# Performance work log

Hardware: AMD Instinct MI355X
Metric: run time of the kernel (lower is better)

Reference implementation:

```python
import jax, jax.numpy as jnp
import numpy as np

N_OBJ, N_REL = 2048, 32768
OBJ_DIM, POOL, H, E, C = 4096, 2048, 512, 200, 151
GEO = 128
IMG_W, IMG_H = 1024.0, 768.0
NUM_ITER = 3


def _lin(x, W, b):
    return x @ W.T + b


def _gru(x, h, Wih, Whh, bih, bhh):
    # torch.nn.GRUCell math; gates stacked (r, z, n)
    gi = x @ Wih.T + bih
    gh = h @ Whh.T + bhh
    i_r, i_z, i_n = jnp.split(gi, 3, axis=-1)
    h_r, h_z, h_n = jnp.split(gh, 3, axis=-1)
    r = jax.nn.sigmoid(i_r + h_r)
    z = jax.nn.sigmoid(i_z + h_z)
    n = jnp.tanh(i_n + r * h_n)
    return (1.0 - z) * n + z * h


def _box_info(boxes, norm=None):
    # [x1,y1,x2,y2,cx,cy,w,h]
    wh = boxes[:, 2:4] - boxes[:, 0:2] + 1.0
    ctr = boxes[:, 0:2] + 0.5 * wh
    info = jnp.concatenate([boxes, ctr, wh], axis=1)
    return info / norm if norm is not None else info


def _box_pair_info(b1, b2):
    # b1,b2: [R,8] normalized box infos -> [R,32]
    ub = jnp.stack([jnp.minimum(b1[:, 0], b2[:, 0]), jnp.minimum(b1[:, 1], b2[:, 1]),
                    jnp.maximum(b1[:, 2], b2[:, 2]), jnp.maximum(b1[:, 3], b2[:, 3])], axis=1)
    ib = jnp.stack([jnp.maximum(b1[:, 0], b2[:, 0]), jnp.maximum(b1[:, 1], b2[:, 1]),
                    jnp.minimum(b1[:, 2], b2[:, 2]), jnp.minimum(b1[:, 3], b2[:, 3])], axis=1)
    inter = _box_info(ib)
    bad = (ib[:, 2] < ib[:, 0]) | (ib[:, 3] < ib[:, 1])
    inter = jnp.where(bad[:, None], 0.0, inter)
    return jnp.concatenate([b1, b2, _box_info(ub), inter], axis=1)


def _encode_box_info(boxes):
    # motifs 9-d geometry encoding
    wh = boxes[:, 2:4] - boxes[:, 0:2] + 1.0
    xy = boxes[:, 0:2] + 0.5 * wh
    w, h = wh[:, 0:1], wh[:, 1:2]
    x, y = xy[:, 0:1], xy[:, 1:2]
    x1, y1, x2, y2 = boxes[:, 0:1], boxes[:, 1:2], boxes[:, 2:3], boxes[:, 3:4]
    return jnp.concatenate([w / IMG_W, h / IMG_H, x / IMG_W, y / IMG_H, x1 / IMG_W,
                            y1 / IMG_H, x2 / IMG_W, y2 / IMG_H, w * h / (IMG_W * IMG_H)], axis=1)


def _forward(inst_roi_feats, union_features, boxes, emb_dist_W, emb_label_W, up_W, up_b,
             pairup_W, pairup_b, pos1_W, pos1_b, bn_g, bn_b, bn_m, bn_v, pos2_W, pos2_b,
             spt1_W, spt1_b, spt2_W, spt2_b, pairfin_W, pairfin_b, objhid_W, objhid_b,
             objfin_W, objfin_b, objU_W, objU_b, edgeU_W, edgeU_b,
             egru_Wih, egru_Whh, egru_bih, egru_bhh, ngru_Wih, ngru_Whh, ngru_bih, ngru_bhh,
             svw_W, svw_b, ovw_W, ovw_b, obj_labels, sub_idx, obj_idx):
    # ---- PairwiseFeatureExtractor ----
    # pos_embed: fc(9,32) -> eval BatchNorm1d(32) -> fc(32,128) -> ReLU
    p = _lin(_encode_box_info(boxes), pos1_W, pos1_b)
    p = (p - bn_m) * bn_g / jnp.sqrt(bn_v + 1e-5) + bn_b
    pos_embed = jax.nn.relu(_lin(p, pos2_W, pos2_b))
    emb_dist = emb_dist_W[obj_labels]                       # predcls: embed GT labels
    aug = _lin(jnp.concatenate([inst_roi_feats, emb_dist, pos_embed], 1), objhid_W, objhid_b)
    augment = jnp.concatenate([emb_label_W[obj_labels], inst_roi_feats, aug], 1)  # [N,4808]
    # pairwise (edge) features: gather head/tail reps + spatial gating
    obox = _box_info(boxes, norm=max(IMG_W, IMG_H, 100.0))  # [N,8]
    fused = _lin(augment, pairup_W, pairup_b).reshape(-1, 2, H)
    pair = jnp.concatenate([fused[:, 0][sub_idx], fused[:, 1][obj_idx]], 1)  # [R,1024]
    geo = _box_pair_info(obox[sub_idx], obox[obj_idx])      # [R,32]
    spt = jax.nn.relu(_lin(jax.nn.relu(_lin(geo, spt1_W, spt1_b)), spt2_W, spt2_b))
    rel_feats = jax.nn.relu(_lin(pair * spt, pairfin_W, pairfin_b))
    rel_feats = rel_feats + _lin(union_features, up_W, up_b)  # 'fusion' + dim-up
    obj_feats = jax.nn.relu(_lin(augment, objfin_W, objfin_b))
    # ---- IMP iterative message passing ----
    obj_rep = _lin(obj_feats, objU_W, objU_b)
    rel_rep = jax.nn.relu(_lin(rel_feats, edgeU_W, edgeU_b))
    vert = _gru(obj_rep, jnp.zeros_like(obj_rep), ngru_Wih, ngru_Whh, ngru_bih, ngru_bhh)
    edge = _gru(rel_rep, jnp.zeros_like(rel_rep), egru_Wih, egru_Whh, egru_bih, egru_bhh)
    n = vert.shape[0]
    for _ in range(NUM_ITER):
        sv, ov = vert[sub_idx], vert[obj_idx]
        ws = jax.nn.sigmoid(_lin(jnp.concatenate([sv, edge], 1), svw_W, svw_b))  # [R,1]
        wo = jax.nn.sigmoid(_lin(jnp.concatenate([ov, edge], 1), ovw_W, ovw_b))
        new_edge = _gru(ws * sv + wo * ov, edge, egru_Wih, egru_Whh, egru_bih, egru_bhh)
        # sub2rel @ (ws*edge) + obj2rel @ (wo*edge) == segment sums over pair indices
        ctx = jax.ops.segment_sum(ws * edge, sub_idx, n) + jax.ops.segment_sum(wo * edge, obj_idx, n)
        vert = _gru(ctx, vert, ngru_Wih, ngru_Whh, ngru_bih, ngru_bhh)
        edge = new_edge
    return vert, edge


def setup_inputs() -> dict:
    keys = jax.random.split(jax.random.key(0), 64)
    ki = iter(keys)

    def nrm(shape, s=0.02):
        return (jax.random.normal(next(ki), shape) * s).astype(jnp.float32)

    kb = jax.random.split(next(ki), 4)
    x1 = jax.random.uniform(kb[0], (N_OBJ,)) * (IMG_W - 200.0)
    y1 = jax.random.uniform(kb[1], (N_OBJ,)) * (IMG_H - 150.0)
    x2 = x1 + 1.0 + jax.random.uniform(kb[2], (N_OBJ,)) * 199.0
    y2 = y1 + 1.0 + jax.random.uniform(kb[3], (N_OBJ,)) * 149.0
    boxes = jnp.stack([x1, y1, x2, y2], axis=1).astype(jnp.float32)

    inp = {
        'inst_roi_feats': nrm((N_OBJ, OBJ_DIM), 1.0),
        'union_features': nrm((N_REL, OBJ_DIM), 1.0),
        'boxes': boxes,
        'emb_dist_W': nrm((C, E)), 'emb_label_W': nrm((C, E)),
        'up_W': nrm((POOL, OBJ_DIM)), 'up_b': jnp.zeros((POOL,), jnp.float32),
        'pairup_W': nrm((2 * H, H + OBJ_DIM + E)), 'pairup_b': jnp.zeros((2 * H,), jnp.float32),
        'pos1_W': nrm((32, 9)), 'pos1_b': jnp.zeros((32,), jnp.float32),
        'bn_g': jnp.ones((32,), jnp.float32), 'bn_b': jnp.zeros((32,), jnp.float32),
        'bn_m': nrm((32,)), 'bn_v': jnp.ones((32,), jnp.float32),
        'pos2_W': nrm((GEO, 32)), 'pos2_b': jnp.zeros((GEO,), jnp.float32),
        'spt1_W': nrm((H, 32)), 'spt1_b': jnp.zeros((H,), jnp.float32),
        'spt2_W': nrm((2 * H, H)), 'spt2_b': jnp.zeros((2 * H,), jnp.float32),
        'pairfin_W': nrm((POOL, 2 * H)), 'pairfin_b': jnp.zeros((POOL,), jnp.float32),
        'objhid_W': nrm((H, OBJ_DIM + E + GEO)), 'objhid_b': jnp.zeros((H,), jnp.float32),
        'objfin_W': nrm((POOL, H + OBJ_DIM + E)), 'objfin_b': jnp.zeros((POOL,), jnp.float32),
        'objU_W': nrm((H, POOL)), 'objU_b': jnp.zeros((H,), jnp.float32),
        'edgeU_W': nrm((H, POOL)), 'edgeU_b': jnp.zeros((H,), jnp.float32),
        'egru_Wih': nrm((3 * H, H)), 'egru_Whh': nrm((3 * H, H)),
        'egru_bih': jnp.zeros((3 * H,), jnp.float32), 'egru_bhh': jnp.zeros((3 * H,), jnp.float32),
        'ngru_Wih': nrm((3 * H, H)), 'ngru_Whh': nrm((3 * H, H)),
        'ngru_bih': jnp.zeros((3 * H,), jnp.float32), 'ngru_bhh': jnp.zeros((3 * H,), jnp.float32),
        'svw_W': nrm((1, 2 * H)), 'svw_b': jnp.zeros((1,), jnp.float32),
        'ovw_W': nrm((1, 2 * H)), 'ovw_b': jnp.zeros((1,), jnp.float32),
        'obj_labels': jax.random.randint(next(ki), (N_OBJ,), 0, C),
        'sub_idx': jax.random.randint(next(ki), (N_REL,), 0, N_OBJ),
        'obj_idx': jax.random.randint(next(ki), (N_REL,), 0, N_OBJ),
    }
    return inp


def reference(inst_roi_feats, union_features, boxes, emb_dist_W, emb_label_W, up_W, up_b,
              pairup_W, pairup_b, pos1_W, pos1_b, bn_g, bn_b, bn_m, bn_v, pos2_W, pos2_b,
              spt1_W, spt1_b, spt2_W, spt2_b, pairfin_W, pairfin_b, objhid_W, objhid_b,
              objfin_W, objfin_b, objU_W, objU_b, edgeU_W, edgeU_b,
              egru_Wih, egru_Whh, egru_bih, egru_bhh, ngru_Wih, ngru_Whh, ngru_bih, ngru_bhh,
              svw_W, svw_b, ovw_W, ovw_b, obj_labels, sub_idx, obj_idx):
    return _forward(inst_roi_feats, union_features, boxes, emb_dist_W, emb_label_W, up_W, up_b,
                    pairup_W, pairup_b, pos1_W, pos1_b, bn_g, bn_b, bn_m, bn_v, pos2_W, pos2_b,
                    spt1_W, spt1_b, spt2_W, spt2_b, pairfin_W, pairfin_b, objhid_W, objhid_b,
                    objfin_W, objfin_b, objU_W, objU_b, edgeU_W, edgeU_b,
                    egru_Wih, egru_Whh, egru_bih, egru_bhh, ngru_Wih, ngru_Whh, ngru_bih, ngru_bhh,
                    svw_W, svw_b, ovw_W, ovw_b, obj_labels, sub_idx, obj_idx)
```

## Files before the change

### kernel.cpp

```cpp
#include <hip/hip_runtime.h>
#include <stdint.h>

#define NOBJ 2048
#define NREL 32768

typedef __attribute__((ext_vector_type(8))) short short8;
typedef __attribute__((ext_vector_type(4))) float f32x4;
typedef __attribute__((ext_vector_type(4))) unsigned short ushort4v;

__device__ __forceinline__ unsigned short f2bs(float x){
  unsigned u = __float_as_uint(x);
  unsigned v = u + 0x7fffu + ((u >> 16) & 1u);
  return (unsigned short)(v >> 16);
}
__device__ __forceinline__ float b2f(unsigned short u){
  return __uint_as_float(((unsigned)u) << 16);
}
__device__ __forceinline__ float sigf(float x){ return 1.0f / (1.0f + expf(-x)); }

__device__ __forceinline__ void gload16(const unsigned short* g, unsigned short* l) {
  __builtin_amdgcn_global_load_lds(
      (const __attribute__((address_space(1))) unsigned int*)(uintptr_t)g,
      (__attribute__((address_space(3))) unsigned int*)(uintptr_t)l,
      16, 0, 0);
}

template<int RMODE, bool ACCUM, bool PRODF>
__global__ __launch_bounds__(512, 2)
void gemm256(const unsigned short* __restrict__ A, const unsigned short* __restrict__ B,
             const float* __restrict__ bias, const float* __restrict__ Cin,
             unsigned short* __restrict__ C, int M, int N, int K, int lda, int ldc,
             const unsigned short* __restrict__ fusedp,
             const int* __restrict__ subp, const int* __restrict__ objp)
{
  __shared__ __align__(16) unsigned short lds[2][2][16384];
  const int t = threadIdx.x;
  const int l = t & 63;
  const int w = t >> 6;
  const int wr = w >> 2, wc = w & 3;
  const int lrow = l & 15, kg = l >> 4;

  const int nwg = gridDim.x;
  const int q8 = nwg >> 3, r8 = nwg & 7;
  const int xcd = blockIdx.x & 7, bidx = blockIdx.x >> 3;
  const int wgid = (xcd < r8 ? xcd * (q8 + 1) : r8 * (q8 + 1) + (xcd - r8) * q8) + bidx;
  const int ntile = N >> 8;
  const int bm = wgid / ntile, bn = wgid - bm * ntile;
  const int m0 = bm << 8, n0 = bn << 8;

  const int srow = w * 8 + (l >> 3);
  const int sel  = ((l & 7) ^ ((l >> 3) & 7)) << 3;
  const unsigned short* Ab0 = A + (long)(m0 + srow) * lda + sel;
  const unsigned short* Bb0 = B + (long)(n0 + srow) * K + sel;
  const long lda64 = (long)64 * lda;
  const long ldb64 = (long)64 * K;
  const int NT = K >> 6;

#define STG256(pA, pB, kt) do { \
    const unsigned short* a_ = Ab0 + (long)(kt) * 64; \
    const unsigned short* b_ = Bb0 + (long)(kt) * 64; \
    gload16(a_,              (pA)); \
    gload16(a_ + lda64,      (pA) + 4096); \
    gload16(a_ + 2 * lda64,  (pA) + 8192); \
    gload16(a_ + 3 * lda64,  (pA) + 12288); \
    gload16(b_,              (pB)); \
    gload16(b_ + ldb64,      (pB) + 4096); \
    gload16(b_ + 2 * ldb64,  (pB) + 8192); \
    gload16(b_ + 3 * ldb64,  (pB) + 12288); \
  } while (0)

  unsigned short* sA0 = &lds[0][0][w * 512];
  unsigned short* sB0 = &lds[0][1][w * 512];
  unsigned short* sA1 = &lds[1][0][w * 512];
  unsigned short* sB1 = &lds[1][1][w * 512];

  f32x4 acc[8][4] = {};

  STG256(sA0, sB0, 0);
  if (NT > 1) STG256(sA1, sB1, 1);

  for (int kt = 0; kt < NT; ++kt) {
    const int cur = kt & 1;
    if (kt + 1 < NT) asm volatile("s_waitcnt vmcnt(8)" ::: "memory");
    else             asm volatile("s_waitcnt vmcnt(0)" ::: "memory");
    __builtin_amdgcn_s_barrier();
    asm volatile("" ::: "memory");

    const unsigned short* As_ = &lds[cur][0][0];
    const unsigned short* Bs_ = &lds[cur][1][0];

    short8 bfr[4][2];
#pragma unroll
    for (int j = 0; j < 4; j++) {
      const int rb = wc * 64 + j * 16 + lrow;
#pragma unroll
      for (int ks = 0; ks < 2; ks++) {
        const int a16 = rb * 8 + ((ks * 4 + kg) ^ (rb & 7));
        bfr[j][ks] = *(const short8*)(Bs_ + a16 * 8);
      }
    }
#pragma unroll
    for (int p = 0; p < 4; p++) {
      short8 afr[2][2];
#pragma unroll
      for (int ii = 0; ii < 2; ii++) {
        const int ra = wr * 128 + (p * 2 + ii) * 16 + lrow;
#pragma unroll
        for (int ks = 0; ks < 2; ks++) {
          const int a16 = ra * 8 + ((ks * 4 + kg) ^ (ra & 7));
          afr[ii][ks] = *(const short8*)(As_ + a16 * 8);
        }
      }
      __builtin_amdgcn_s_setprio(1);
#pragma unroll
      for (int ii = 0; ii < 2; ii++)
#pragma unroll
        for (int j = 0; j < 4; j++)
#pragma unroll
          for (int ks = 0; ks < 2; ks++)
            acc[p * 2 + ii][j] = __builtin_amdgcn_mfma_f32_16x16x32_bf16(
                afr[ii][ks], bfr[j][ks], acc[p * 2 + ii][j], 0, 0, 0);
      __builtin_amdgcn_s_setprio(0);
    }
    asm volatile("" ::: "memory");
    __builtin_amdgcn_s_barrier();
    asm volatile("" ::: "memory");
    if (kt + 2 < NT) {
      unsigned short* pa = (cur == 0) ? sA0 : sA1;
      unsigned short* pb = (cur == 0) ? sB0 : sB1;
      STG256(pa, pb, kt + 2);
    }
  }
#undef STG256

#pragma unroll
  for (int i = 0; i < 8; i++) {
#pragma unroll
    for (int j = 0; j < 4; j++) {
      const int col = n0 + wc * 64 + j * 16 + lrow;
      const float bv = bias[col];
#pragma unroll
      for (int q = 0; q < 4; q++) {
        const long row = m0 + wr * 128 + i * 16 + kg * 4 + q;
        float v = acc[i][j][q] + bv;
        if constexpr (RMODE == 1) v = fmaxf(v, 0.0f);
        if constexpr (PRODF) {
          int gr = (col < 512) ? subp[row] : objp[row];
          v *= b2f(fusedp[(long)gr * 1024 + col]);
        }
        if constexpr (ACCUM) v += Cin[row * (long)N + col];
        if constexpr (RMODE == 2) v = fmaxf(v, 0.0f);
        C[row * (long)ldc + col] = f2bs(v);
      }
    }
  }
}

template<int RMODE, bool ACCUM, bool OUTB, bool PRODF, bool AF32>
__global__ __launch_bounds__(256, 2)
void gemm_bt(const void* __restrict__ Ap, const unsigned short* __restrict__ B,
             const float* __restrict__ bias, const float* __restrict__ Cin,
             void* __restrict__ Cp, int M, int N, int K, int lda, int ldc,
             const unsigned short* __restrict__ fusedp,
             const int* __restrict__ subp, const int* __restrict__ objp)
{
  __shared__ __align__(16) unsigned short As[128 * 32];
  __shared__ __align__(16) unsigned short Bs[128 * 32];
  const int t = threadIdx.x;
  const int lane = t & 63;
  const int w = t >> 6;
  const int nwg = gridDim.x;
  const int q8 = nwg >> 3, r8 = nwg & 7;
  const int xcd = blockIdx.x & 7, bidx = blockIdx.x >> 3;
  const int wgid = (xcd < r8 ? xcd * (q8 + 1) : r8 * (q8 + 1) + (xcd - r8) * q8) + bidx;
  const int ntile = N >> 7;
  const int bm = wgid / ntile;
  const int bn = wgid - bm * ntile;
  const int m0 = bm << 7, n0 = bn << 7;
  const int wm = (w & 1) << 6, wn = (w >> 1) << 6;
  const int lrow = lane & 15, kg = lane >> 4;

  const int c0 = w << 1;
  const int srow = (c0 << 4) + (lane >> 2);
  const int selem = (((lane & 3) ^ ((lane >> 3) & 3)) << 3);
  const unsigned short* bg0 = B + (long)(n0 + srow) * K + selem;
  const unsigned short* bg1 = bg0 + (long)16 * K;
// ... 64 lines not shown
#pragma unroll
  for (int i = 0; i < 4; i++) {
#pragma unroll
    for (int j = 0; j < 4; j++) {
      const int col = n0 + wn + j * 16 + lrow;
      const float bv = bias[col];
#pragma unroll
      for (int q = 0; q < 4; q++) {
        const long row = m0 + wm + i * 16 + kg * 4 + q;
        float v = acc[i][j][q] + bv;
        if constexpr (RMODE == 1) v = fmaxf(v, 0.0f);
        if constexpr (PRODF) {
          int gr = (col < 512) ? subp[row] : objp[row];
          v *= b2f(fusedp[(long)gr * 1024 + col]);
        }
        if constexpr (ACCUM) v += Cin[row * (long)N + col];
        if constexpr (RMODE == 2) v = fmaxf(v, 0.0f);
        if constexpr (OUTB) Cb[row * (long)ldc + col] = f2bs(v);
        else Cf[row * (long)ldc + col] = v;
      }
    }
  }
}


__global__ void cvt_pad4(const float* __restrict__ src, unsigned short* __restrict__ dst,
                         int rows, int K0, int Kp)
{
  const int kp4 = Kp >> 2;
  const long total = (long)rows * kp4;
  for (long i = blockIdx.x * (long)blockDim.x + threadIdx.x; i < total; i += (long)gridDim.x * blockDim.x) {
    int r = (int)(i / kp4), k = (int)(i - (long)r * kp4) << 2;
    ushort4v o;
    if (k < K0) {
      f32x4 v = *(const f32x4*)(src + (long)r * K0 + k);
      o[0] = f2bs(v[0]); o[1] = f2bs(v[1]); o[2] = f2bs(v[2]); o[3] = f2bs(v[3]);
    } else {
      o[0] = 0; o[1] = 0; o[2] = 0; o[3] = 0;
    }
    *(ushort4v*)(dst + (long)r * Kp + k) = o;
  }
}

__global__ void cvt4(const float* __restrict__ src, unsigned short* __restrict__ dst, long n4)
{
  for (long i = blockIdx.x * (long)blockDim.x + threadIdx.x; i < n4; i += (long)gridDim.x * blockDim.x) {
    f32x4 v = ((const f32x4*)src)[i];
    ushort4v o;
    o[0] = f2bs(v[0]); o[1] = f2bs(v[1]); o[2] = f2bs(v[2]); o[3] = f2bs(v[3]);
    ((ushort4v*)dst)[i] = o;
  }
}

__global__ void build_wcat(const float* __restrict__ wih, const float* __restrict__ whh,
                           unsigned short* __restrict__ dst)
{
  const long total = 1024L * 256;
  for (long i = blockIdx.x * (long)blockDim.x + threadIdx.x; i < total; i += (long)gridDim.x * blockDim.x) {
    int j = (int)(i >> 8), k = ((int)(i & 255)) << 2;
    const float* s = (k < 512) ? (wih + (long)j * 512 + k) : (whh + (long)j * 512 + (k - 512));
    f32x4 v = *(const f32x4*)s;
    ushort4v o;
    o[0] = f2bs(v[0]); o[1] = f2bs(v[1]); o[2] = f2bs(v[2]); o[3] = f2bs(v[3]);
    *(ushort4v*)(dst + (long)j * 1024 + k) = o;
  }
}

__global__ void bias_rz_k(const float* __restrict__ bih, const float* __restrict__ bhh,
                          float* __restrict__ out)
{
  int j = blockIdx.x * blockDim.x + threadIdx.x;
  if (j < 1024) out[j] = bih[j] + bhh[j];
}

__global__ void transpose_cvt(const float* __restrict__ src, unsigned short* __restrict__ dst,
                              int R, int C)
{
  __shared__ float tile[32][33];
  int c0 = blockIdx.x * 32, r0 = blockIdx.y * 32;
  for (int i = threadIdx.y; i < 32; i += 8)
    tile[i][threadIdx.x] = src[(long)(r0 + i) * C + c0 + threadIdx.x];
  __syncthreads();
  for (int i = threadIdx.y; i < 32; i += 8)
    dst[(long)(c0 + i) * R + r0 + threadIdx.x] = f2bs(tile[threadIdx.x][i]);
}

__global__ void comp_bias(const float* __restrict__ edgeU_W, const float* __restrict__ up_b,
                          const float* __restrict__ edgeU_b, float* __restrict__ b_comp)
{
  int j = (int)((blockIdx.x * (long)blockDim.x + threadIdx.x) >> 6);
  int l = threadIdx.x & 63;
  if (j >= 512) return;
  float s = 0.0f;
  for (int k = l; k < 2048; k += 64) s += edgeU_W[(long)j * 2048 + k] * up_b[k];
#pragma unroll
  for (int off = 32; off > 0; off >>= 1) s += __shfl_xor(s, off);
  if (l == 0) b_comp[j] = s + edgeU_b[j];
}

__global__ void obox_k(const float* __restrict__ boxes, float* __restrict__ obox)
{
  int i = blockIdx.x * blockDim.x + threadIdx.x;
  if (i >= NOBJ) return;
  float x1 = boxes[i*4], y1 = boxes[i*4+1], x2 = boxes[i*4+2], y2 = boxes[i*4+3];
  float wdt = x2 - x1 + 1.0f, hgt = y2 - y1 + 1.0f;
  float cx = x1 + 0.5f * wdt, cy = y1 + 0.5f * hgt;
  const float inv = 1.0f / 1024.0f;
  float* o = obox + i * 8;
  o[0]=x1*inv; o[1]=y1*inv; o[2]=x2*inv; o[3]=y2*inv;
  o[4]=cx*inv; o[5]=cy*inv; o[6]=wdt*inv; o[7]=hgt*inv;
}

__global__ void posembed_k(const float* __restrict__ boxes,
                           const float* __restrict__ w1, const float* __restrict__ b1,
                           const float* __restrict__ g, const float* __restrict__ bb,
                           const float* __restrict__ mm, const float* __restrict__ vv,
                           const float* __restrict__ w2, const float* __restrict__ b2,
                           float* __restrict__ out)
{
  int o = blockIdx.x, t = threadIdx.x;
  __shared__ float e[9];
  __shared__ float p[32];
  if (t == 0) {
    float x1 = boxes[o*4], y1 = boxes[o*4+1], x2 = boxes[o*4+2], y2 = boxes[o*4+3];
    float wdt = x2 - x1 + 1.0f, hgt = y2 - y1 + 1.0f;
    float cx = x1 + 0.5f * wdt, cy = y1 + 0.5f * hgt;
    e[0]=wdt/1024.0f; e[1]=hgt/768.0f; e[2]=cx/1024.0f; e[3]=cy/768.0f;
// ... 99 lines not shown
    const unsigned short* gr = gi + (long)r * 1536;
    short8 vr = *(const short8*)(gr + c);
    short8 vz = *(const short8*)(gr + 512 + c);
    short8 vn = *(const short8*)(gr + 1024 + c);
    float hv[8];
#pragma unroll
    for (int k = 0; k < 8; k++) {
      float rr = sigf(b2f((unsigned short)vr[k]) + bhh[c + k]);
      float z  = sigf(b2f((unsigned short)vz[k]) + bhh[512 + c + k]);
      float nn = tanhf(b2f((unsigned short)vn[k]) + rr * bhh[1024 + c + k]);
      hv[k] = (1.0f - z) * nn;
    }
    float* hp = h + (long)r * 512 + c;
    *(f32x4*)hp = *(f32x4*)hv;
    *(f32x4*)(hp + 4) = *(f32x4*)(hv + 4);
    pack8_store(hb + (long)r * hstride + c, *(f32x4*)hv, *(f32x4*)(hv + 4));
  }
}

__global__ void gru_step_v(const unsigned short* __restrict__ gi, const unsigned short* __restrict__ gh,
                           const float* __restrict__ hin, float* __restrict__ hout,
                           unsigned short* __restrict__ hb, int n)
{
  const long total = (long)n * 64;
  for (long i = blockIdx.x * (long)blockDim.x + threadIdx.x; i < total; i += (long)gridDim.x * blockDim.x) {
    int r = (int)(i >> 6), c = ((int)(i & 63)) << 3;
    const unsigned short* gr = gi + (long)r * 1536;
    const unsigned short* hr = gh + (long)r * 1536;
    short8 ir = *(const short8*)(gr + c);
    short8 iz = *(const short8*)(gr + 512 + c);
    short8 in_ = *(const short8*)(gr + 1024 + c);
    short8 hrr = *(const short8*)(hr + c);
    short8 hz = *(const short8*)(hr + 512 + c);
    short8 hn = *(const short8*)(hr + 1024 + c);
    const float* hi = hin + (long)r * 512 + c;
    f32x4 h0 = *(const f32x4*)hi;
    f32x4 h1 = *(const f32x4*)(hi + 4);
    float hv[8];
#pragma unroll
    for (int k = 0; k < 8; k++) {
      float rr = sigf(b2f((unsigned short)ir[k]) + b2f((unsigned short)hrr[k]));
      float z  = sigf(b2f((unsigned short)iz[k]) + b2f((unsigned short)hz[k]));
      float nn = tanhf(b2f((unsigned short)in_[k]) + rr * b2f((unsigned short)hn[k]));
      float old = (k < 4) ? h0[k] : h1[k - 4];
      hv[k] = (1.0f - z) * nn + z * old;
    }
    float* hp = hout + (long)r * 512 + c;
    *(f32x4*)hp = *(f32x4*)hv;
    *(f32x4*)(hp + 4) = *(f32x4*)(hv + 4);
    pack8_store(hb + (long)r * 512 + c, *(f32x4*)hv, *(f32x4*)(hv + 4));
  }
}

__global__ void gru_step_e(const unsigned short* __restrict__ gates,
                           const float* __restrict__ hin, float* __restrict__ hout,
                           unsigned short* __restrict__ xe, int n)
{
  const long total = (long)n * 64;
  for (long i = blockIdx.x * (long)blockDim.x + threadIdx.x; i < total; i += (long)gridDim.x * blockDim.x) {
    int r = (int)(i >> 6), c = ((int)(i & 63)) << 3;
    const unsigned short* g = gates + (long)r * 2048;
    short8 vr = *(const short8*)(g + c);
    short8 vz = *(const short8*)(g + 512 + c);
    short8 vi = *(const short8*)(g + 1024 + c);
    short8 vh = *(const short8*)(g + 1536 + c);
    const float* hi = hin + (long)r * 512 + c;
    f32x4 h0 = *(const f32x4*)hi;
    f32x4 h1 = *(const f32x4*)(hi + 4);
    float hv[8];
#pragma unroll
    for (int k = 0; k < 8; k++) {
      float rr = sigf(b2f((unsigned short)vr[k]));
      float z  = sigf(b2f((unsigned short)vz[k]));
      float nn = tanhf(b2f((unsigned short)vi[k]) + rr * b2f((unsigned short)vh[k]));
      float old = (k < 4) ? h0[k] : h1[k - 4];
      hv[k] = (1.0f - z) * nn + z * old;
    }
    float* hp = hout + (long)r * 512 + c;
    *(f32x4*)hp = *(f32x4*)hv;
    *(f32x4*)(hp + 4) = *(f32x4*)(hv + 4);
    pack8_store(xe + (long)r * 1024 + 512 + c, *(f32x4*)hv, *(f32x4*)(hv + 4));
  }
}

__global__ __launch_bounds__(256)
void edge_weights(const unsigned short* __restrict__ vertb, unsigned short* __restrict__ xe,
                  const int* __restrict__ sub, const int* __restrict__ obj,
                  const float* __restrict__ svwW, const float* __restrict__ svwb,
                  const float* __restrict__ ovwW, const float* __restrict__ ovwb,
                  float* __restrict__ ws_arr, float* __restrict__ wo_arr)
{
  long gid = blockIdx.x * (long)blockDim.x + threadIdx.x;
  int r = (int)(gid >> 6);
  int l = (int)(gid & 63);
  if (r >= NREL) return;
  int s = sub[r], o = obj[r];
  const unsigned short* sv = vertb + (long)s * 512;
  const unsigned short* ov = vertb + (long)o * 512;
  const unsigned short* e  = xe + (long)r * 1024 + 512;
  float svv[8], ovv[8], ev[8];
  float as = 0.0f, ao = 0.0f;
#pragma unroll
  for (int k = 0; k < 8; k++) {
    int c = l + k * 64;
    svv[k] = b2f(sv[c]); ovv[k] = b2f(ov[c]); ev[k] = b2f(e[c]);
    as += svwW[c] * svv[k] + svwW[512 + c] * ev[k];
    ao += ovwW[c] * ovv[k] + ovwW[512 + c] * ev[k];
  }
#pragma unroll
  for (int off = 32; off > 0; off >>= 1) {
    as += __shfl_xor(as, off);
    ao += __shfl_xor(ao, off);
  }
  float ws = sigf(as + svwb[0]);
  float wo = sigf(ao + ovwb[0]);
  unsigned short* xr = xe + (long)r * 1024;
#pragma unroll
  for (int k = 0; k < 8; k++) {
    int c = l + k * 64;
    xr[c] = f2bs(ws * svv[k] + wo * ovv[k]);
  }
  if (l == 0) { ws_arr[r] = ws; wo_arr[r] = wo; }
}


__global__ void csr_count(const int* __restrict__ sub, const int* __restrict__ obj,
                          int* __restrict__ cnt)
{
  int r = blockIdx.x * blockDim.x + threadIdx.x;
  if (r >= NREL) return;
  atomicAdd(&cnt[sub[r]], 1);
  atomicAdd(&cnt[obj[r]], 1);
}

__global__ __launch_bounds__(1024)
void csr_scan(const int* __restrict__ cnt, int* __restrict__ off)
{
  __shared__ int a[1024], b[1024];
  int t = threadIdx.x;
  int c0 = cnt[2*t], c1 = cnt[2*t+1];
  a[t] = c0 + c1;
  __syncthreads();
  int* src = a; int* dst = b;
  for (int s = 1; s < 1024; s <<= 1) {
    int v = src[t];
    if (t >= s) v += src[t - s];
    dst[t] = v;
    __syncthreads();
    int* tmp = src; src = dst; dst = tmp;
  }
  int incl = src[t];
  int excl = incl - (c0 + c1);
  off[2*t] = excl;
  off[2*t+1] = excl + c0;
  if (t == 1023) off[2048] = incl;
}

__global__ void csr_fill(const int* __restrict__ sub, const int* __restrict__ obj,
                         const int* __restrict__ off, int* __restrict__ rcur,
                         int* __restrict__ lists)
{
  int r = blockIdx.x * blockDim.x + threadIdx.x;
  if (r >= NREL) return;
  int s = sub[r];
  int p = atomicAdd(&rcur[s], 1);
  lists[off[s] + p] = (r << 1);
  int o = obj[r];
  int q = atomicAdd(&rcur[o], 1);
  lists[off[o] + q] = (r << 1) | 1;
}

__global__ __launch_bounds__(128)
void ctx_gather(const unsigned short* __restrict__ xe, const float* __restrict__ ws,
                const float* __restrict__ wo, const int* __restrict__ off,
                const int* __restrict__ lists, unsigned short* __restrict__ ctxb)
{
  __shared__ float part[512];
  int o = blockIdx.x;
  int l = threadIdx.x & 63;
  int w = threadIdx.x >> 6;
  int i0 = off[o], i1 = off[o + 1];
  float acc[8] = {0.f,0.f,0.f,0.f,0.f,0.f,0.f,0.f};
  for (int i = i0 + w; i < i1; i += 2) {
    int e = lists[i];
    int r = e >> 1;
    float sc = (e & 1) ? wo[r] : ws[r];
    short8 row = *(const short8*)(xe + (long)r * 1024 + 512 + l * 8);
#pragma unroll
    for (int k = 0; k < 8; k++) acc[k] += sc * b2f((unsigned short)row[k]);
  }
  if (w == 1) {
    *(f32x4*)&part[l*8]     = *(f32x4*)&acc[0];
    *(f32x4*)&part[l*8 + 4] = *(f32x4*)&acc[4];
  }
  __syncthreads();
  if (w == 0) {
#pragma unroll
    for (int k = 0; k < 8; k++) acc[k] += part[l*8 + k];
    pack8_store(ctxb + (long)o * 512 + l * 8, *(f32x4*)&acc[0], *(f32x4*)&acc[4]);
  }
}


static inline int nblk(long total) {
  long b = (total + 255) / 256;
  return (int)(b > 16384 ? 16384 : b);
}

#define GEMM(RM, AC, OB, PF, grid, Aa, Bb, bb, Ci, Cc, Mm, Nn, Kk, ldA, ldC, fp, sp, op) \
  gemm_bt<RM, AC, OB, PF, false><<<grid, 256, 0, stream>>>(Aa, Bb, bb, Ci, Cc, Mm, Nn, Kk, ldA, ldC, fp, sp, op)
#define GEMMF(RM, AC, OB, grid, Aa, Bb, bb, Ci, Cc, Mm, Nn, Kk, ldA, ldC) \
  gemm_bt<RM, AC, OB, false, true><<<grid, 256, 0, stream>>>(Aa, Bb, bb, Ci, Cc, Mm, Nn, Kk, ldA, ldC, nullptr, nullptr, nullptr)
#define G256(RM, AC, PF, Aa, Bb, bb, Ci, Cc, Mm, Nn, Kk, ldA, ldC, fp, sp, op) \
  gemm256<RM, AC, PF><<<dim3(((Mm) >> 8) * ((Nn) >> 8)), 512, 0, stream>>>(Aa, Bb, bb, Ci, Cc, Mm, Nn, Kk, ldA, ldC, fp, sp, op)

extern "C" void kernel_launch(void* const* d_in, const int* in_sizes, int n_in,
                              void* d_out, int out_size, void* d_ws, size_t ws_size,
                              hipStream_t stream)
{
  const float* inst     = (const float*)d_in[0];
  const float* unionf   = (const float*)d_in[1];
  const float* boxes    = (const float*)d_in[2];
  const float* embd_W   = (const float*)d_in[3];
  const float* embl_W   = (const float*)d_in[4];
  const float* up_W     = (const float*)d_in[5];
  const float* up_b     = (const float*)d_in[6];
  const float* pairup_W = (const float*)d_in[7];
  const float* pairup_b = (const float*)d_in[8];
  const float* pos1_W   = (const float*)d_in[9];
  const float* pos1_b   = (const float*)d_in[10];
  const float* bn_g     = (const float*)d_in[11];
  const float* bn_b     = (const float*)d_in[12];
  const float* bn_m     = (const float*)d_in[13];
  const float* bn_v     = (const float*)d_in[14];
  const float* pos2_W   = (const float*)d_in[15];
  const float* pos2_b   = (const float*)d_in[16];
  const float* spt1_W   = (const float*)d_in[17];
  const float* spt1_b   = (const float*)d_in[18];
  const float* spt2_W   = (const float*)d_in[19];
  const float* spt2_b   = (const float*)d_in[20];
  const float* pairfin_W= (const float*)d_in[21];
  const float* pairfin_b= (const float*)d_in[22];
  const float* objhid_W = (const float*)d_in[23];
  const float* objhid_b = (const float*)d_in[24];
  const float* objfin_W = (const float*)d_in[25];
  const float* objfin_b = (const float*)d_in[26];
  const float* objU_W   = (const float*)d_in[27];
  const float* objU_b   = (const float*)d_in[28];
  const float* edgeU_W  = (const float*)d_in[29];
  const float* edgeU_b  = (const float*)d_in[30];
  const float* egru_Wih = (const float*)d_in[31];
  const float* egru_Whh = (const float*)d_in[32];
  const float* egru_bih = (const float*)d_in[33];
  const float* egru_bhh = (const float*)d_in[34];
  const float* ngru_Wih = (const float*)d_in[35];
  const float* ngru_Whh = (const float*)d_in[36];
  const float* ngru_bih = (const float*)d_in[37];
  const float* ngru_bhh = (const float*)d_in[38];
  const float* svw_W    = (const float*)d_in[39];
  const float* svw_b    = (const float*)d_in[40];
  const float* ovw_W    = (const float*)d_in[41];
  const float* ovw_b    = (const float*)d_in[42];
  const int*   labels   = (const int*)d_in[43];
  const int*   sub      = (const int*)d_in[44];
  const int*   obj      = (const int*)d_in[45];
  (void)in_sizes; (void)n_in; (void)out_size; (void)ws_size;

  char* base = (char*)d_ws;
  size_t off = 0;
  auto alloc = [&](size_t bytes) -> void* {
    void* p = base + off;
    off += (bytes + 255) & ~(size_t)255;
    return p;
  };

  unsigned short* objhid_Wb  = (unsigned short*)alloc(512L  * 4480 * 2);
  unsigned short* pairup_Wb  = (unsigned short*)alloc(1024L * 4864 * 2);
  unsigned short* objfin_Wb  = (unsigned short*)alloc(2048L * 4864 * 2);
  unsigned short* up_Wtb     = (unsigned short*)alloc(4096L * 2048 * 2);
  unsigned short* pairfin_Wb = (unsigned short*)alloc(2048L * 1024 * 2);
  unsigned short* spt1_Wb    = (unsigned short*)alloc(512L  * 64   * 2);
  unsigned short* spt2_Wb    = (unsigned short*)alloc(1024L * 512  * 2);
  unsigned short* objU_Wb    = (unsigned short*)alloc(512L  * 2048 * 2);
  unsigned short* edgeU_Wb   = (unsigned short*)alloc(512L  * 2048 * 2);
  unsigned short* egru_Wihb  = (unsigned short*)alloc(1536L * 512  * 2);
  unsigned short* egru_Whhb  = (unsigned short*)alloc(1536L * 512  * 2);
  unsigned short* ngru_Wihb  = (unsigned short*)alloc(1536L * 512  * 2);
  unsigned short* ngru_Whhb  = (unsigned short*)alloc(1536L * 512  * 2);
  unsigned short* Wcat_rzb   = (unsigned short*)alloc(1024L * 1024 * 2);
  unsigned short* W_compb    = (unsigned short*)alloc(512L  * 4096 * 2);
  float*          b_comp     = (float*)alloc(512L * 4);
  float*          zbias      = (float*)alloc(4096L * 4);
  float*          bias_rz    = (float*)alloc(1024L * 4);

  float*          obox      = (float*)alloc(NOBJ * 8L * 4);
  float*          pose      = (float*)alloc(NOBJ * 128L * 4);
  unsigned short* obj_featsb= (unsigned short*)alloc((long)NOBJ * 2048 * 2);
  unsigned short* obj_repb  = (unsigned short*)alloc((long)NOBJ * 512 * 2);
  unsigned short* giv       = (unsigned short*)alloc((long)NOBJ * 1536 * 2);
  unsigned short* ghv       = (unsigned short*)alloc((long)NOBJ * 1536 * 2);
  float*          vert      = (float*)alloc((long)NOBJ * 512 * 4);
  unsigned short* vertb     = (unsigned short*)alloc((long)NOBJ * 512 * 2);
  unsigned short* ctxb      = (unsigned short*)alloc((long)NOBJ * 512 * 2);
  unsigned short* geob      = (unsigned short*)alloc((long)NREL * 64 * 2);
  float*          edge      = (float*)alloc((long)NREL * 512 * 4);
  unsigned short* xe        = (unsigned short*)alloc((long)NREL * 1024 * 2);
  float*          ws_arr    = (float*)alloc((long)NREL * 4);
  float*          wo_arr    = (float*)alloc((long)NREL * 4);

  int* cnt   = (int*)alloc(NOBJ * 4);
  int* coff  = (int*)alloc((NOBJ + 1) * 4);
  int* rcur  = (int*)alloc(NOBJ * 4);
  int* lists = (int*)alloc(2L * NREL * 4);

  char* regA = (char*)alloc((long)NREL * 512 * 4);
  unsigned short* X1b = (unsigned short*)regA;
  float*          T1  = (float*)regA;
  char* regB = (char*)alloc((long)NOBJ * 4864 * 2 > (long)NREL * 512 * 2
                            ? (long)NOBJ * 4864 * 2 : (long)NREL * 512 * 2);
  unsigned short* augb     = (unsigned short*)regB;
  unsigned short* rel_repb = (unsigned short*)regB;
  unsigned short* fusedb = (unsigned short*)alloc((long)NOBJ * 1024 * 2);
  unsigned short* spt1b  = (unsigned short*)alloc((long)NREL * 512 * 2);
  char* big1 = (char*)alloc((long)NREL * 1536 * 4);
  unsigned short* G1    = (unsigned short*)big1;
  unsigned short* prodb = (unsigned short*)(big1 + (long)NREL * 1024 * 4);
  unsigned short* gi_e  = (unsigned short*)big1;
  unsigned short* gates = (unsigned short*)big1;

  float* d_out_vert = (float*)d_out;
  float* d_out_edge = (float*)d_out + (long)NOBJ * 512;

  cvt_pad4<<<nblk(512L*4480/4),  256, 0, stream>>>(objhid_W,  objhid_Wb,  512,  4424, 4480);
  cvt_pad4<<<nblk(1024L*4864/4), 256, 0, stream>>>(pairup_W,  pairup_Wb,  1024, 4808, 4864);
  cvt_pad4<<<nblk(2048L*4864/4), 256, 0, stream>>>(objfin_W,  objfin_Wb,  2048, 4808, 4864);
  cvt_pad4<<<nblk(512L*64/4),    256, 0, stream>>>(spt1_W,    spt1_Wb,    512,  32,   64);
  cvt4<<<nblk(2048L*1024/4), 256, 0, stream>>>(pairfin_W, pairfin_Wb, 2048L*1024/4);
  cvt4<<<nblk(1024L*512/4),  256, 0, stream>>>(spt2_W,    spt2_Wb,    1024L*512/4);
  cvt4<<<nblk(512L*2048/4),  256, 0, stream>>>(objU_W,    objU_Wb,    512L*2048/4);
  cvt4<<<nblk(512L*2048/4),  256, 0, stream>>>(edgeU_W,   edgeU_Wb,   512L*2048/4);
  cvt4<<<nblk(1536L*512/4),  256, 0, stream>>>(egru_Wih,  egru_Wihb,  1536L*512/4);
  cvt4<<<nblk(1536L*512/4),  256, 0, stream>>>(egru_Whh,  egru_Whhb,  1536L*512/4);
  cvt4<<<nblk(1536L*512/4),  256, 0, stream>>>(ngru_Wih,  ngru_Wihb,  1536L*512/4);
  cvt4<<<nblk(1536L*512/4),  256, 0, stream>>>(ngru_Whh,  ngru_Whhb,  1536L*512/4);
  build_wcat<<<nblk(1024L*256), 256, 0, stream>>>(egru_Wih, egru_Whh, Wcat_rzb);
  bias_rz_k<<<4, 256, 0, stream>>>(egru_bih, egru_bhh, bias_rz);
  transpose_cvt<<<dim3(4096/32, 2048/32), dim3(32, 8), 0, stream>>>(up_W, up_Wtb, 2048, 4096);
  hipMemsetAsync(zbias, 0, 4096L * 4, stream);
  comp_bias<<<128, 256, 0, stream>>>(edgeU_W, up_b, edgeU_b, b_comp);
  GEMM(0,false,true,false, dim3((512>>7)*(4096>>7)), edgeU_Wb, up_Wtb, zbias, nullptr, W_compb, 512, 4096, 2048, 2048, 4096, nullptr, nullptr, nullptr);

  hipMemsetAsync(cnt, 0, NOBJ * 4, stream);
  hipMemsetAsync(rcur, 0, NOBJ * 4, stream);
  csr_count<<<NREL/256, 256, 0, stream>>>(sub, obj, cnt);
  csr_scan<<<1, 1024, 0, stream>>>(cnt, coff);
  csr_fill<<<NREL/256, 256, 0, stream>>>(sub, obj, coff, rcur, lists);

  obox_k<<<(NOBJ + 255) / 256, 256, 0, stream>>>(boxes, obox);
  posembed_k<<<NOBJ, 128, 0, stream>>>(boxes, pos1_W, pos1_b, bn_g, bn_b, bn_m, bn_v,
                                       pos2_W, pos2_b, pose);
  build_x1<<<nblk((long)NOBJ*560), 256, 0, stream>>>(inst, embd_W, labels, pose, X1b);
  build_aug<<<nblk((long)NOBJ*608), 256, 0, stream>>>(embl_W, labels, inst, augb);
  GEMM(0,false,true ,false, dim3((NOBJ>>7)*(512>>7)),  X1b, objhid_Wb, objhid_b, nullptr, augb + 4296, NOBJ, 512, 4480, 4480, 4864, nullptr, nullptr, nullptr);
  GEMM(0,false,true ,false, dim3((NOBJ>>7)*(1024>>7)), augb, pairup_Wb, pairup_b, nullptr, fusedb, NOBJ, 1024, 4864, 4864, 1024, nullptr, nullptr, nullptr);
  GEMM(1,false,true ,false, dim3((NOBJ>>7)*(2048>>7)), augb, objfin_Wb, objfin_b, nullptr, obj_featsb, NOBJ, 2048, 4864, 4864, 2048, nullptr, nullptr, nullptr);
  GEMM(0,false,true ,false, dim3((NOBJ>>7)*(512>>7)),  obj_featsb, objU_Wb, objU_b, nullptr, obj_repb, NOBJ, 512, 2048, 2048, 512, nullptr, nullptr, nullptr);
  GEMM(0,false,true ,false, dim3((NOBJ>>7)*(1536>>7)), obj_repb, ngru_Wihb, ngru_bih, nullptr, giv, NOBJ, 1536, 512, 512, 1536, nullptr, nullptr, nullptr);
  gru_init<<<nblk((long)NOBJ*64), 256, 0, stream>>>(giv, ngru_bhh, vert, vertb, 512, NOBJ);

  build_geo<<<(NREL + 255) / 256, 256, 0, stream>>>(obox, sub, obj, geob);
  GEMM(1,false,true ,false, dim3((NREL>>7)*(512>>7)),  geob, spt1_Wb, spt1_b, nullptr, spt1b, NREL, 512, 64, 64, 512, nullptr, nullptr, nullptr);
  G256(1,false,true , spt1b, spt2_Wb, spt2_b, nullptr, prodb, NREL, 1024, 512, 512, 1024, fusedb, sub, obj);
  G256(1,false,false, prodb, pairfin_Wb, pairfin_b, nullptr, G1, NREL, 2048, 1024, 1024, 2048, nullptr, nullptr, nullptr);
  GEMMF(0,false,false, dim3((NREL>>7)*(512>>7)), unionf, W_compb, b_comp, nullptr, T1, NREL, 512, 4096, 4096, 512);
  G256(2,true ,false, G1, edgeU_Wb, zbias, T1, rel_repb, NREL, 512, 2048, 2048, 512, nullptr, nullptr, nullptr);
  G256(0,false,false, rel_repb, egru_Wihb, egru_bih, nullptr, gi_e, NREL, 1536, 512, 512, 1536, nullptr, nullptr, nullptr);
  gru_init<<<nblk((long)NREL*64), 256, 0, stream>>>(gi_e, egru_bhh, edge, xe + 512, 1024, NREL);

  for (int it = 0; it < 3; it++) {
    const bool last = (it == 2);
    edge_weights<<<(NREL * 64) / 256, 256, 0, stream>>>(vertb, xe, sub, obj,
                                                        svw_W, svw_b, ovw_W, ovw_b, ws_arr, wo_arr);
    ctx_gather<<<NOBJ, 128, 0, stream>>>(xe, ws_arr, wo_arr, coff, lists, ctxb);
    G256(0,false,false, xe,       Wcat_rzb,              bias_rz,        nullptr, gates,        NREL, 1024, 1024, 1024, 2048, nullptr, nullptr, nullptr);
    G256(0,false,false, xe,       egru_Wihb + 1024L*512, egru_bih + 1024, nullptr, gates + 1024, NREL, 512,  512,  1024, 2048, nullptr, nullptr, nullptr);
    G256(0,false,false, xe + 512, egru_Whhb + 1024L*512, egru_bhh + 1024, nullptr, gates + 1536, NREL, 512,  512,  1024, 2048, nullptr, nullptr, nullptr);
    GEMM(0,false,true,false, dim3((NOBJ>>7)*(1536>>7)), ctxb,  ngru_Wihb, ngru_bih, nullptr, giv, NOBJ, 1536, 512, 512, 1536, nullptr, nullptr, nullptr);
    GEMM(0,false,true,false, dim3((NOBJ>>7)*(1536>>7)), vertb, ngru_Whhb, ngru_bhh, nullptr, ghv, NOBJ, 1536, 512, 512, 1536, nullptr, nullptr, nullptr);
    gru_step_e<<<nblk((long)NREL*64), 256, 0, stream>>>(gates, edge, last ? d_out_edge : edge, xe, NREL);
    gru_step_v<<<nblk((long)NOBJ*64), 256, 0, stream>>>(giv, ghv, vert, last ? d_out_vert : vert, vertb, NOBJ);
  }
}
```

Baseline: 2.059 ms.

## Factor edge GRU input projection through vertex features; triple-buffer 256 GEMM K-loop

The edge GRU input ws*v_sub + wo*v_obj is linear, so its projection is now computed once per object (2048-row GEMM into VWb) and then combined per edge inside the GRU step kernel. This removes the per-edge 1024-wide input GEMM and the materialized mixed input. It also drops the concatenated Wcat weights and the xe buffer. Separately, the 256x256 GEMM now uses K-steps of 32 with a three-stage LDS ring and a single barrier per step, issuing the next load before the MFMAs. The per-edge step now does two random gathers of 1536-wide vertex rows, and it rounds the per-object projection to bf16 before mixing, which changes numerics slightly.

Measured after the change: 2.014 ms. -2.2%, faster.

```diff
diff --git a/kernel.cpp b/kernel.cpp
--- a/kernel.cpp
+++ b/kernel.cpp
@@ -33,7 +33,7 @@
              const unsigned short* __restrict__ fusedp,
              const int* __restrict__ subp, const int* __restrict__ objp)
 {
-  __shared__ __align__(16) unsigned short lds[2][2][16384];
+  __shared__ __align__(16) unsigned short lds[3][2][8192];
   const int t = threadIdx.x;
   const int l = t & 63;
   const int w = t >> 6;
@@ -48,40 +48,33 @@
   const int bm = wgid / ntile, bn = wgid - bm * ntile;
   const int m0 = bm << 8, n0 = bn << 8;
 
-  const int srow = w * 8 + (l >> 3);
-  const int sel  = ((l & 7) ^ ((l >> 3) & 7)) << 3;
-  const unsigned short* Ab0 = A + (long)(m0 + srow) * lda + sel;
-  const unsigned short* Bb0 = B + (long)(n0 + srow) * K + sel;
-  const long lda64 = (long)64 * lda;
-  const long ldb64 = (long)64 * K;
-  const int NT = K >> 6;
-
-#define STG256(pA, pB, kt) do { \
-    const unsigned short* a_ = Ab0 + (long)(kt) * 64; \
-    const unsigned short* b_ = Bb0 + (long)(kt) * 64; \
-    gload16(a_,              (pA)); \
-    gload16(a_ + lda64,      (pA) + 4096); \
-    gload16(a_ + 2 * lda64,  (pA) + 8192); \
-    gload16(a_ + 3 * lda64,  (pA) + 12288); \
-    gload16(b_,              (pB)); \
-    gload16(b_ + ldb64,      (pB) + 4096); \
-    gload16(b_ + 2 * ldb64,  (pB) + 8192); \
-    gload16(b_ + 3 * ldb64,  (pB) + 12288); \
+  const int sel = ((l & 3) ^ ((l >> 3) & 3)) << 3;
+  const unsigned short* Ag = A + (long)(m0 + w * 32 + (l >> 2)) * lda + sel;
+  const unsigned short* Bg = B + (long)(n0 + w * 32 + (l >> 2)) * K + sel;
+  const long lda16 = (long)16 * lda;
+  const long ldb16 = (long)16 * K;
+  const int NT = K >> 5;
+
+#define STG(tile) do { \
+    const int bsel = (tile) % 3; \
+    unsigned short* pA = &lds[bsel][0][w * 1024]; \
+    unsigned short* pB = &lds[bsel][1][w * 1024]; \
+    const unsigned short* a_ = Ag + (long)(tile) * 32; \
+    const unsigned short* b_ = Bg + (long)(tile) * 32; \
+    gload16(a_,         pA); \
+    gload16(a_ + lda16, pA + 512); \
+    gload16(b_,         pB); \
+    gload16(b_ + ldb16, pB + 512); \
   } while (0)
 
-  unsigned short* sA0 = &lds[0][0][w * 512];
-  unsigned short* sB0 = &lds[0][1][w * 512];
-  unsigned short* sA1 = &lds[1][0][w * 512];
-  unsigned short* sB1 = &lds[1][1][w * 512];
-
   f32x4 acc[8][4] = {};
 
-  STG256(sA0, sB0, 0);
-  if (NT > 1) STG256(sA1, sB1, 1);
+  STG(0);
+  if (NT > 1) STG(1);
 
   for (int kt = 0; kt < NT; ++kt) {
-    const int cur = kt & 1;
-    if (kt + 1 < NT) asm volatile("s_waitcnt vmcnt(8)" ::: "memory");
+    const int cur = kt % 3;
+    if (kt + 1 < NT) asm volatile("s_waitcnt vmcnt(4)" ::: "memory");
     else             asm volatile("s_waitcnt vmcnt(0)" ::: "memory");
     __builtin_amdgcn_s_barrier();
     asm volatile("" ::: "memory");
@@ -89,49 +82,29 @@
     const unsigned short* As_ = &lds[cur][0][0];
     const unsigned short* Bs_ = &lds[cur][1][0];
 
-    short8 bfr[4][2];
+    short8 bfr[4];
 #pragma unroll
     for (int j = 0; j < 4; j++) {
       const int rb = wc * 64 + j * 16 + lrow;
-#pragma unroll
-      for (int ks = 0; ks < 2; ks++) {
-        const int a16 = rb * 8 + ((ks * 4 + kg) ^ (rb & 7));
-        bfr[j][ks] = *(const short8*)(Bs_ + a16 * 8);
-      }
-    }
-#pragma unroll
-    for (int p = 0; p < 4; p++) {
-      short8 afr[2][2];
-#pragma unroll
-      for (int ii = 0; ii < 2; ii++) {
-        const int ra = wr * 128 + (p * 2 + ii) * 16 + lrow;
-#pragma unroll
-        for (int ks = 0; ks < 2; ks++) {
-          const int a16 = ra * 8 + ((ks * 4 + kg) ^ (ra & 7));
-          afr[ii][ks] = *(const short8*)(As_ + a16 * 8);
-        }
-      }
-      __builtin_amdgcn_s_setprio(1);
-#pragma unroll
-      for (int ii = 0; ii < 2; ii++)
-#pragma unroll
-        for (int j = 0; j < 4; j++)
-#pragma unroll
-          for (int ks = 0; ks < 2; ks++)
-            acc[p * 2 + ii][j] = __builtin_amdgcn_mfma_f32_16x16x32_bf16(
-                afr[ii][ks], bfr[j][ks], acc[p * 2 + ii][j], 0, 0, 0);
-      __builtin_amdgcn_s_setprio(0);
-    }
+      bfr[j] = *(const short8*)(Bs_ + rb * 32 + ((kg ^ ((rb >> 1) & 3)) << 3));
+    }
+    short8 afr[8];
+#pragma unroll
+    for (int i = 0; i < 8; i++) {
+      const int ra = wr * 128 + i * 16 + lrow;
+      afr[i] = *(const short8*)(As_ + ra * 32 + ((kg ^ ((ra >> 1) & 3)) << 3));
+    }
+    if (kt + 2 < NT) STG(kt + 2);
+    __builtin_amdgcn_s_setprio(1);
+#pragma unroll
+    for (int i = 0; i < 8; i++)
+#pragma unroll
+      for (int j = 0; j < 4; j++)
+        acc[i][j] = __builtin_amdgcn_mfma_f32_16x16x32_bf16(afr[i], bfr[j], acc[i][j], 0, 0, 0);
+    __builtin_amdgcn_s_setprio(0);
     asm volatile("" ::: "memory");
-    __builtin_amdgcn_s_barrier();
-    asm volatile("" ::: "memory");
-    if (kt + 2 < NT) {
-      unsigned short* pa = (cur == 0) ? sA0 : sA1;
-      unsigned short* pb = (cur == 0) ? sB0 : sB1;
-      STG256(pa, pb, kt + 2);
-    }
-  }
-#undef STG256
+  }
+#undef STG
 
 #pragma unroll
   for (int i = 0; i < 8; i++) {
@@ -302,27 +275,6 @@
   }
 }
 
-__global__ void build_wcat(const float* __restrict__ wih, const float* __restrict__ whh,
-                           unsigned short* __restrict__ dst)
-{
-  const long total = 1024L * 256;
-  for (long i = blockIdx.x * (long)blockDim.x + threadIdx.x; i < total; i += (long)gridDim.x * blockDim.x) {
-    int j = (int)(i >> 8), k = ((int)(i & 255)) << 2;
-    const float* s = (k < 512) ? (wih + (long)j * 512 + k) : (whh + (long)j * 512 + (k - 512));
-    f32x4 v = *(const f32x4*)s;
-    ushort4v o;
-    o[0] = f2bs(v[0]); o[1] = f2bs(v[1]); o[2] = f2bs(v[2]); o[3] = f2bs(v[3]);
-    *(ushort4v*)(dst + (long)j * 1024 + k) = o;
-  }
-}
-
-__global__ void bias_rz_k(const float* __restrict__ bih, const float* __restrict__ bhh,
-                          float* __restrict__ out)
-{
-  int j = blockIdx.x * blockDim.x + threadIdx.x;
-  if (j < 1024) out[j] = bih[j] + bhh[j];
-}
-
 __global__ void transpose_cvt(const float* __restrict__ src, unsigned short* __restrict__ dst,
                               int R, int C)
 {
@@ -528,39 +480,55 @@
   }
 }
 
-__global__ void gru_step_e(const unsigned short* __restrict__ gates,
-                           const float* __restrict__ hin, float* __restrict__ hout,
-                           unsigned short* __restrict__ xe, int n)
+__global__ void gru_step_e2(const unsigned short* __restrict__ GH,
+                            const unsigned short* __restrict__ VW,
+                            const float* __restrict__ ws_arr, const float* __restrict__ wo_arr,
+                            const int* __restrict__ sub, const int* __restrict__ obj,
+                            const float* __restrict__ bih,
+                            const float* __restrict__ hin, float* __restrict__ hout,
+                            unsigned short* __restrict__ hb, int n)
 {
   const long total = (long)n * 64;
   for (long i = blockIdx.x * (long)blockDim.x + threadIdx.x; i < total; i += (long)gridDim.x * blockDim.x) {
     int r = (int)(i >> 6), c = ((int)(i & 63)) << 3;
-    const unsigned short* g = gates + (long)r * 2048;
-    short8 vr = *(const short8*)(g + c);
-    short8 vz = *(const short8*)(g + 512 + c);
-    short8 vi = *(const short8*)(g + 1024 + c);
-    short8 vh = *(const short8*)(g + 1536 + c);
+    int s = sub[r], o = obj[r];
+    float ws = ws_arr[r], wo = wo_arr[r];
+    const unsigned short* gh = GH + (long)r * 1536;
+    const unsigned short* vs = VW + (long)s * 1536;
+    const unsigned short* vo = VW + (long)o * 1536;
+    short8 ghr = *(const short8*)(gh + c);
+    short8 ghz = *(const short8*)(gh + 512 + c);
+    short8 ghn = *(const short8*)(gh + 1024 + c);
+    short8 vsr = *(const short8*)(vs + c);
+    short8 vsz = *(const short8*)(vs + 512 + c);
+    short8 vsn = *(const short8*)(vs + 1024 + c);
+    short8 vor_ = *(const short8*)(vo + c);
+    short8 voz = *(const short8*)(vo + 512 + c);
+    short8 von = *(const short8*)(vo + 1024 + c);
     const float* hi = hin + (long)r * 512 + c;
     f32x4 h0 = *(const f32x4*)hi;
     f32x4 h1 = *(const f32x4*)(hi + 4);
     float hv[8];
 #pragma unroll
     for (int k = 0; k < 8; k++) {
-      float rr = sigf(b2f((unsigned short)vr[k]));
-      float z  = sigf(b2f((unsigned short)vz[k]));
-      float nn = tanhf(b2f((unsigned short)vi[k]) + rr * b2f((unsigned short)vh[k]));
+      float gir = ws * b2f((unsigned short)vsr[k]) + wo * b2f((unsigned short)vor_[k]) + bih[c + k];
+      float giz = ws * b2f((unsigned short)vsz[k]) + wo * b2f((unsigned short)voz[k]) + bih[512 + c + k];
+      float gin = ws * b2f((unsigned short)vsn[k]) + wo * b2f((unsigned short)von[k]) + bih[1024 + c + k];
+      float rr = sigf(gir + b2f((unsigned short)ghr[k]));
+      float z  = sigf(giz + b2f((unsigned short)ghz[k]));
+      float nn = tanhf(gin + rr * b2f((unsigned short)ghn[k]));
       float old = (k < 4) ? h0[k] : h1[k - 4];
       hv[k] = (1.0f - z) * nn + z * old;
     }
     float* hp = hout + (long)r * 512 + c;
     *(f32x4*)hp = *(f32x4*)hv;
     *(f32x4*)(hp + 4) = *(f32x4*)(hv + 4);
-    pack8_store(xe + (long)r * 1024 + 512 + c, *(f32x4*)hv, *(f32x4*)(hv + 4));
+    pack8_store(hb + (long)r * 512 + c, *(f32x4*)hv, *(f32x4*)(hv + 4));
   }
 }
 
 __global__ __launch_bounds__(256)
-void edge_weights(const unsigned short* __restrict__ vertb, unsigned short* __restrict__ xe,
+void edge_weights(const unsigned short* __restrict__ vertb, const unsigned short* __restrict__ edgeb,
                   const int* __restrict__ sub, const int* __restrict__ obj,
                   const float* __restrict__ svwW, const float* __restrict__ svwb,
                   const float* __restrict__ ovwW, const float* __restrict__ ovwb,
@@ -573,30 +541,24 @@
   int s = sub[r], o = obj[r];
   const unsigned short* sv = vertb + (long)s * 512;
   const unsigned short* ov = vertb + (long)o * 512;
-  const unsigned short* e  = xe + (long)r * 1024 + 512;
-  float svv[8], ovv[8], ev[8];
+  const unsigned short* e  = edgeb + (long)r * 512;
   float as = 0.0f, ao = 0.0f;
 #pragma unroll
   for (int k = 0; k < 8; k++) {
     int c = l + k * 64;
-    svv[k] = b2f(sv[c]); ovv[k] = b2f(ov[c]); ev[k] = b2f(e[c]);
-    as += svwW[c] * svv[k] + svwW[512 + c] * ev[k];
-    ao += ovwW[c] * ovv[k] + ovwW[512 + c] * ev[k];
+    float svv = b2f(sv[c]), ovv = b2f(ov[c]), ev = b2f(e[c]);
+    as += svwW[c] * svv + svwW[512 + c] * ev;
+    ao += ovwW[c] * ovv + ovwW[512 + c] * ev;
   }
 #pragma unroll
   for (int off = 32; off > 0; off >>= 1) {
     as += __shfl_xor(as, off);
     ao += __shfl_xor(ao, off);
   }
-  float ws = sigf(as + svwb[0]);
-  float wo = sigf(ao + ovwb[0]);
-  unsigned short* xr = xe + (long)r * 1024;
-#pragma unroll
-  for (int k = 0; k < 8; k++) {
-    int c = l + k * 64;
-    xr[c] = f2bs(ws * svv[k] + wo * ovv[k]);
-  }
-  if (l == 0) { ws_arr[r] = ws; wo_arr[r] = wo; }
+  if (l == 0) {
+    ws_arr[r] = sigf(as + svwb[0]);
+    wo_arr[r] = sigf(ao + ovwb[0]);
+  }
 }
 
 
@@ -647,7 +609,7 @@
 }
 
 __global__ __launch_bounds__(128)
-void ctx_gather(const unsigned short* __restrict__ xe, const float* __restrict__ ws,
+void ctx_gather(const unsigned short* __restrict__ edgeb, const float* __restrict__ ws,
                 const float* __restrict__ wo, const int* __restrict__ off,
                 const int* __restrict__ lists, unsigned short* __restrict__ ctxb)
 {
@@ -661,7 +623,7 @@
     int e = lists[i];
     int r = e >> 1;
     float sc = (e & 1) ? wo[r] : ws[r];
-    short8 row = *(const short8*)(xe + (long)r * 1024 + 512 + l * 8);
+    short8 row = *(const short8*)(edgeb + (long)r * 512 + l * 8);
 #pragma unroll
     for (int k = 0; k < 8; k++) acc[k] += sc * b2f((unsigned short)row[k]);
   }
@@ -763,11 +725,9 @@
   unsigned short* egru_Whhb  = (unsigned short*)alloc(1536L * 512  * 2);
   unsigned short* ngru_Wihb  = (unsigned short*)alloc(1536L * 512  * 2);
   unsigned short* ngru_Whhb  = (unsigned short*)alloc(1536L * 512  * 2);
-  unsigned short* Wcat_rzb   = (unsigned short*)alloc(1024L * 1024 * 2);
   unsigned short* W_compb    = (unsigned short*)alloc(512L  * 4096 * 2);
   float*          b_comp     = (float*)alloc(512L * 4);
   float*          zbias      = (float*)alloc(4096L * 4);
-  float*          bias_rz    = (float*)alloc(1024L * 4);
 
   float*          obox      = (float*)alloc(NOBJ * 8L * 4);
   float*          pose      = (float*)alloc(NOBJ * 128L * 4);
@@ -775,12 +735,13 @@
   unsigned short* obj_repb  = (unsigned short*)alloc((long)NOBJ * 512 * 2);
   unsigned short* giv       = (unsigned short*)alloc((long)NOBJ * 1536 * 2);
   unsigned short* ghv       = (unsigned short*)alloc((long)NOBJ * 1536 * 2);
+  unsigned short* VWb       = (unsigned short*)alloc((long)NOBJ * 1536 * 2);
   float*          vert      = (float*)alloc((long)NOBJ * 512 * 4);
   unsigned short* vertb     = (unsigned short*)alloc((long)NOBJ * 512 * 2);
   unsigned short* ctxb      = (unsigned short*)alloc((long)NOBJ * 512 * 2);
   unsigned short* geob      = (unsigned short*)alloc((long)NREL * 64 * 2);
   float*          edge      = (float*)alloc((long)NREL * 512 * 4);
-  unsigned short* xe        = (unsigned short*)alloc((long)NREL * 1024 * 2);
+  unsigned short* edgeb     = (unsigned short*)alloc((long)NREL * 512 * 2);
   float*          ws_arr    = (float*)alloc((long)NREL * 4);
   float*          wo_arr    = (float*)alloc((long)NREL * 4);
 
@@ -802,7 +763,7 @@
   unsigned short* G1    = (unsigned short*)big1;
   unsigned short* prodb = (unsigned short*)(big1 + (long)NREL * 1024 * 4);
   unsigned short* gi_e  = (unsigned short*)big1;
-  unsigned short* gates = (unsigned short*)big1;
+  unsigned short* GHb   = (unsigned short*)big1;
 
   float* d_out_vert = (float*)d_out;
   float* d_out_edge = (float*)d_out + (long)NOBJ * 512;
@@ -819,8 +780,6 @@
   cvt4<<<nblk(1536L*512/4),  256, 0, stream>>>(egru_Whh,  egru_Whhb,  1536L*512/4);
   cvt4<<<nblk(1536L*512/4),  256, 0, stream>>>(ngru_Wih,  ngru_Wihb,  1536L*512/4);
   cvt4<<<nblk(1536L*512/4),  256, 0, stream>>>(ngru_Whh,  ngru_Whhb,  1536L*512/4);
-  build_wcat<<<nblk(1024L*256), 256, 0, stream>>>(egru_Wih, egru_Whh, Wcat_rzb);
-  bias_rz_k<<<4, 256, 0, stream>>>(egru_bih, egru_bhh, bias_rz);
   transpose_cvt<<<dim3(4096/32, 2048/32), dim3(32, 8), 0, stream>>>(up_W, up_Wtb, 2048, 4096);
   hipMemsetAsync(zbias, 0, 4096L * 4, stream);
   comp_bias<<<128, 256, 0, stream>>>(edgeU_W, up_b, edgeU_b, b_comp);
@@ -851,19 +810,19 @@
   GEMMF(0,false,false, dim3((NREL>>7)*(512>>7)), unionf, W_compb, b_comp, nullptr, T1, NREL, 512, 4096, 4096, 512);
   G256(2,true ,false, G1, edgeU_Wb, zbias, T1, rel_repb, NREL, 512, 2048, 2048, 512, nullptr, nullptr, nullptr);
   G256(0,false,false, rel_repb, egru_Wihb, egru_bih, nullptr, gi_e, NREL, 1536, 512, 512, 1536, nullptr, nullptr, nullptr);
-  gru_init<<<nblk((long)NREL*64), 256, 0, stream>>>(gi_e, egru_bhh, edge, xe + 512, 1024, NREL);
+  gru_init<<<nblk((long)NREL*64), 256, 0, stream>>>(gi_e, egru_bhh, edge, edgeb, 512, NREL);
 
   for (int it = 0; it < 3; it++) {
     const bool last = (it == 2);
-    edge_weights<<<(NREL * 64) / 256, 256, 0, stream>>>(vertb, xe, sub, obj,
+    edge_weights<<<(NREL * 64) / 256, 256, 0, stream>>>(vertb, edgeb, sub, obj,
                                                         svw_W, svw_b, ovw_W, ovw_b, ws_arr, wo_arr);
-    ctx_gather<<<NOBJ, 128, 0, stream>>>(xe, ws_arr, wo_arr, coff, lists, ctxb);
-    G256(0,false,false, xe,       Wcat_rzb,              bias_rz,        nullptr, gates,        NREL, 1024, 1024, 1024, 2048, nullptr, nullptr, nullptr);
-    G256(0,false,false, xe,       egru_Wihb + 1024L*512, egru_bih + 1024, nullptr, gates + 1024, NREL, 512,  512,  1024, 2048, nullptr, nullptr, nullptr);
-    G256(0,false,false, xe + 512, egru_Whhb + 1024L*512, egru_bhh + 1024, nullptr, gates + 1536, NREL, 512,  512,  1024, 2048, nullptr, nullptr, nullptr);
+    ctx_gather<<<NOBJ, 128, 0, stream>>>(edgeb, ws_arr, wo_arr, coff, lists, ctxb);
+    GEMM(0,false,true,false, dim3((NOBJ>>7)*(1536>>7)), vertb, egru_Wihb, zbias, nullptr, VWb, NOBJ, 1536, 512, 512, 1536, nullptr, nullptr, nullptr);
+    G256(0,false,false, edgeb, egru_Whhb, egru_bhh, nullptr, GHb, NREL, 1536, 512, 512, 1536, nullptr, nullptr, nullptr);
     GEMM(0,false,true,false, dim3((NOBJ>>7)*(1536>>7)), ctxb,  ngru_Wihb, ngru_bih, nullptr, giv, NOBJ, 1536, 512, 512, 1536, nullptr, nullptr, nullptr);
     GEMM(0,false,true,false, dim3((NOBJ>>7)*(1536>>7)), vertb, ngru_Whhb, ngru_bhh, nullptr, ghv, NOBJ, 1536, 512, 512, 1536, nullptr, nullptr, nullptr);
-    gru_step_e<<<nblk((long)NREL*64), 256, 0, stream>>>(gates, edge, last ? d_out_edge : edge, xe, NREL);
+    gru_step_e2<<<nblk((long)NREL*64), 256, 0, stream>>>(GHb, VWb, ws_arr, wo_arr, sub, obj,
+                                                         egru_bih, edge, last ? d_out_edge : edge, edgeb, NREL);
     gru_step_v<<<nblk((long)NOBJ*64), 256, 0, stream>>>(giv, ghv, vert, last ? d_out_vert : vert, vertb, NOBJ);
   }
 }
```
